# Kernel optimization log

Hardware: AMD Instinct MI355X
Metric: run time of the kernel (lower is better)

## Reference

```python
import jax, jax.numpy as jnp
import numpy as np

B, T, D, H = 2, 2048, 2048, 16
HD = D // H  # head dim = 128


def setup_inputs() -> dict:
    key = jax.random.key(0)
    k_x, k_qkv, k_out, k_doc = jax.random.split(key, 4)
    x = jax.random.normal(k_x, (B, T, D), dtype=jnp.float32)
    # real RoPE tables (sin/cos of position * inv_freq), shape (T, HD)
    inv_freq = 1.0 / (10000.0 ** (jnp.arange(0, HD, 2, dtype=jnp.float32) / HD))
    ang = jnp.arange(T, dtype=jnp.float32)[:, None] * inv_freq[None, :]  # (T, HD/2)
    ang = jnp.concatenate([ang, ang], axis=-1)  # (T, HD)
    sin, cos = jnp.sin(ang), jnp.cos(ang)
    W_qkv = jax.random.normal(k_qkv, (D, 3 * D), dtype=jnp.float32) * 0.02
    W_out = jax.random.normal(k_out, (D, D), dtype=jnp.float32) * 0.02
    # sorted doc ids per row -> contiguous packed documents
    doc_ids = jnp.sort(jax.random.randint(k_doc, (B, T), 0, 8), axis=-1).astype(jnp.int32)
    return {"x": x, "sin": sin, "cos": cos, "W_qkv": W_qkv, "W_out": W_out, "doc_ids": doc_ids}


def _apply_rope(xh, sin, cos):
    # xh: (B, T, H, HD); sin/cos: (T, HD) broadcast over batch & heads
    s = sin[None, :, None, :]
    c = cos[None, :, None, :]
    x1, x2 = jnp.split(xh, 2, axis=-1)
    rot = jnp.concatenate([-x2, x1], axis=-1)  # rotate_half
    return xh * c + rot * s


def reference(x, sin, cos, W_qkv, W_out, doc_ids):
    b, t, d = x.shape
    qkv = x @ W_qkv  # (B, T, 3D), fused QKV projection, no bias
    q, k, v = jnp.split(qkv, 3, axis=-1)
    q = q.reshape(b, t, H, HD)
    k = k.reshape(b, t, H, HD)
    v = v.reshape(b, t, H, HD)
    q = _apply_rope(q, sin, cos)
    k = _apply_rope(k, sin, cos)
    # doc-causal additive bias: (B, 1, T, T)
    neg_inf = jnp.finfo(q.dtype).min / 2
    causal = jnp.tril(jnp.ones((t, t), dtype=jnp.bool_))
    same_doc = doc_ids[:, :, None] == doc_ids[:, None, :]
    mask = (causal[None, :, :] & same_doc)[:, None, :, :]
    bias = jnp.where(mask, 0.0, neg_inf).astype(q.dtype)
    # attention (matches jax.nn.dot_product_attention with additive bias)
    scale = 1.0 / jnp.sqrt(jnp.asarray(HD, dtype=q.dtype))
    scores = jnp.einsum("bqhd,bkhd->bhqk", q, k) * scale + bias
    attn = jax.nn.softmax(scores, axis=-1)
    out = jnp.einsum("bhqk,bkhd->bqhd", attn, v)  # (B, T, H, HD)
    out = out.reshape(b, t, d)
    return out @ W_out
```

## Files before the change

kernel.cpp:

```cpp
#include <hip/hip_runtime.h>
#include <hip/hip_bf16.h>

#define BB 2
#define TT 2048
#define DD 2048
#define HH 16
#define HDIM 128
#define BT 4096
#define N3 6144

typedef __attribute__((ext_vector_type(8))) short s16x8;
typedef __attribute__((ext_vector_type(4))) float f32x4;

static __device__ __forceinline__ ushort f2bf(float x) {
  union { float f; unsigned u; } cv; cv.f = x;
  unsigned r = cv.u + 0x7FFF + ((cv.u >> 16) & 1);
  return (ushort)(r >> 16);
}
static __device__ __forceinline__ float bf2f(ushort u) {
  union { unsigned u; float f; } cv; cv.u = ((unsigned)u) << 16; return cv.f;
}

#define GLDS16(gp, lp) __builtin_amdgcn_global_load_lds( \
    (const __attribute__((address_space(1))) void*)(gp), \
    (__attribute__((address_space(3))) void*)(lp), 16, 0, 0)

__global__ void cvt_kernel(const float* __restrict__ in, ushort* __restrict__ out, int n4) {
  int i = blockIdx.x * blockDim.x + threadIdx.x;
  if (i < n4) {
    float4 v = ((const float4*)in)[i];
    ushort4 o;
    o.x = f2bf(v.x); o.y = f2bf(v.y); o.z = f2bf(v.z); o.w = f2bf(v.w);
    ((ushort4*)out)[i] = o;
  }
}

__global__ void transpose_cvt(const float* __restrict__ in, ushort* __restrict__ out, int R, int C) {
  __shared__ float tile[32][33];
  const int bx = blockIdx.x * 32, by = blockIdx.y * 32;
  const int tx = threadIdx.x, ty = threadIdx.y;
  #pragma unroll
  for (int i = 0; i < 32; i += 8)
    tile[ty + i][tx] = in[(size_t)(by + ty + i) * C + bx + tx];
  __syncthreads();
  #pragma unroll
  for (int i = 0; i < 32; i += 8)
    out[(size_t)(bx + ty + i) * R + by + tx] = f2bf(tile[tx][ty + i]);
}

__global__ __launch_bounds__(512, 1)
void gemm8_qkv(const ushort* __restrict__ A, const ushort* __restrict__ Bt,
               ushort* __restrict__ Qb, ushort* __restrict__ Kb, ushort* __restrict__ Vb)
{
  constexpr int K = 2048;
  constexpr int NT = K / 64;
  constexpr int NBX = N3 / 256;
  constexpr int NWG = NBX * (BT / 256);
  __shared__ char smem[131072];

  const int tid = threadIdx.x, wave = tid >> 6, lane = tid & 63;
  const int lr = lane & 15, lg = lane >> 4;
  const int wm = wave >> 2, wn = wave & 3;

  const int wg = blockIdx.x;
  const int nw = (wg & 7) * (NWG / 8) + (wg >> 3);
  const int by = nw / NBX, bx = nw - by * NBX;
  const int m0 = by * 256, n0 = bx * 256;

  auto STAGE = [&](int s) {
    if (s >= 4 * NT) return;
    const int U = s >> 2, j = s & 3;
    const int ab = j & 1, ks = j >> 1;
    const ushort* src = ab ? Bt : A;
    const int base0 = ab ? n0 : m0;
    char* dst = smem + (((U & 1) << 16) | (ab << 15) | (ks << 14));
    #pragma unroll
    for (int inst = 0; inst < 2; ++inst) {
      const int c = inst * 512 + tid;
      const int row = c >> 2;
      const int colb = (c & 3) * 16;
      const int colsw = colb ^ (((row >> 2) & 3) << 4);
      const ushort* gp = src + (size_t)(base0 + row) * K + U * 64 + ks * 32 + (colsw >> 1);
      GLDS16(gp, dst + inst * 8192 + wave * 1024);
    }
  };

  f32x4 acc[8][4] = {};

  #pragma unroll
  for (int s = 0; s < 6; ++s) STAGE(s);
  asm volatile("s_waitcnt vmcnt(8)" ::: "memory");
  __builtin_amdgcn_s_barrier();

  for (int T = 0; T < NT; ++T) {
    const int buf = T & 1;
    s16x8 a[8];
    #pragma unroll
    for (int p = 0; p < 4; ++p) {
      const int ks = p >> 1, qn = p & 1;
      const char* Ab = smem + ((buf << 16) | (ks << 14));
      const char* Bb = smem + ((buf << 16) | 32768 | (ks << 14));
      if ((p & 1) == 0) {
        #pragma unroll
        for (int mf = 0; mf < 8; ++mf) {
          const int row = wm * 128 + mf * 16 + lr;
          a[mf] = *(const s16x8*)(Ab + row * 64 + ((lg * 16) ^ (((row >> 2) & 3) << 4)));
        }
      }
      s16x8 bb[2];
      #pragma unroll
      for (int nf = 0; nf < 2; ++nf) {
        const int row = wn * 64 + qn * 32 + nf * 16 + lr;
        bb[nf] = *(const s16x8*)(Bb + row * 64 + ((lg * 16) ^ (((row >> 2) & 3) << 4)));
      }
      STAGE(4 * T + p + 6);
      if (p & 1) asm volatile("s_waitcnt vmcnt(8)" ::: "memory");
      __builtin_amdgcn_s_barrier();
      asm volatile("s_waitcnt lgkmcnt(0)" ::: "memory");
      __builtin_amdgcn_sched_barrier(0);
      __builtin_amdgcn_s_setprio(1);
      #pragma unroll
      for (int mf = 0; mf < 8; ++mf)
        #pragma unroll
        for (int nf = 0; nf < 2; ++nf)
          acc[mf][qn * 2 + nf] =
            __builtin_amdgcn_mfma_f32_16x16x32_bf16(a[mf], bb[nf], acc[mf][qn * 2 + nf], 0, 0, 0);
      __builtin_amdgcn_s_setprio(0);
      __builtin_amdgcn_s_barrier();
    }
  }

  #pragma unroll
  for (int mf = 0; mf < 8; ++mf) {
    #pragma unroll
    for (int nn = 0; nn < 4; ++nn) {
      #pragma unroll
      for (int r = 0; r < 4; ++r) {
        const int rowg = m0 + wm * 128 + mf * 16 + lg * 4 + r;
        const int colg = n0 + wn * 64 + nn * 16 + lr;
        const int which = colg >> 11, rem = colg & 2047;
        const int hh = rem >> 7, d = rem & 127;
        const int b2 = rowg >> 11, t = rowg & 2047;
        ushort* dstp = (which == 0) ? Qb : (which == 1) ? Kb : Vb;
        dstp[(((size_t)b2 * HH + hh) * TT + t) * HDIM + d] = f2bf(acc[mf][nn][r]);
      }
    }
  }
}

__global__ __launch_bounds__(256, 2)
void gemm_bt2(const ushort* __restrict__ A, const ushort* __restrict__ Bt,
              float* __restrict__ Cf, int M, int N, int K)
{
  __shared__ ushort As[128 * 32];
  __shared__ ushort Bs[128 * 32];
  const int tid = threadIdx.x;
  const int wave = tid >> 6, lane = tid & 63;
  const int lr = lane & 15, lg = lane >> 4;
  const int m0 = blockIdx.y * 128, n0 = blockIdx.x * 128;
  const int wm = (wave & 1) * 64, wn = (wave >> 1) * 64;
  f32x4 acc[4][4] = {};

  for (int k0 = 0; k0 < K; k0 += 32) {
    __syncthreads();
    #pragma unroll
    for (int call = 0; call < 2; ++call) {
      const int base = call * 256 + wave * 64;
      const int c = base + lane;
      const int row = c >> 2, cc = c & 3;
      GLDS16(A  + (size_t)(m0 + row) * K + k0 + cc * 8, As + (size_t)base * 8);
      GLDS16(Bt + (size_t)(n0 + row) * K + k0 + cc * 8, Bs + (size_t)base * 8);
    }
    __syncthreads();
    s16x8 a[4], b[4];
    #pragma unroll
    for (int i = 0; i < 4; ++i) a[i] = *(const s16x8*)&As[(wm + i * 16 + lr) * 32 + lg * 8];
    #pragma unroll
    for (int i = 0; i < 4; ++i) b[i] = *(const s16x8*)&Bs[(wn + i * 16 + lr) * 32 + lg * 8];
    #pragma unroll
    for (int mi = 0; mi < 4; ++mi)
      #pragma unroll
      for (int ni = 0; ni < 4; ++ni)
        acc[mi][ni] = __builtin_amdgcn_mfma_f32_16x16x32_bf16(a[mi], b[ni], acc[mi][ni], 0, 0, 0);
  }

  #pragma unroll
  for (int mi = 0; mi < 4; ++mi)
    #pragma unroll
    for (int ni = 0; ni < 4; ++ni)
      #pragma unroll
      for (int r = 0; r < 4; ++r) {
        const int row = m0 + wm + mi * 16 + lg * 4 + r;
        const int col = n0 + wn + ni * 16 + lr;
        Cf[(size_t)row * N + col] = acc[mi][ni][r];
      }
}

__global__ void rope_inplace(ushort* __restrict__ Qb, ushort* __restrict__ Kb,
                             const float* __restrict__ sinp, const float* __restrict__ cosp) {
  const int idx = blockIdx.x * 256 + threadIdx.x;
  const int d = idx & 63;
  const int t = (idx >> 6) & (TT - 1);
  const int bh = idx >> 17;
  const float c = cosp[t * HDIM + d];
  const float s = sinp[t * HDIM + d];
  const size_t base = ((size_t)bh * TT + t) * HDIM + d;
  float q1 = bf2f(Qb[base]), q2 = bf2f(Qb[base + 64]);
  Qb[base]      = f2bf(q1 * c - q2 * s);
  Qb[base + 64] = f2bf(q2 * c + q1 * s);
  float k1 = bf2f(Kb[base]), k2 = bf2f(Kb[base + 64]);
  Kb[base]      = f2bf(k1 * c - k2 * s);
  Kb[base + 64] = f2bf(k2 * c + k1 * s);
}

__global__ __launch_bounds__(256, 2)
void attn_kernel(const ushort* __restrict__ Qb, const ushort* __restrict__ Kb,
                 const ushort* __restrict__ Vb, const int* __restrict__ doc,
                 ushort* __restrict__ Ob)
{
  __shared__ ushort Ks[64 * 128];
  __shared__ ushort VTs[128 * 64];
  __shared__ ushort Ps[4][16 * 64];
  const int qt = blockIdx.x, h = blockIdx.y, b = blockIdx.z;
  const int q0 = qt * 64;
  const int tid = threadIdx.x, wave = tid >> 6, lane = tid & 63;
  const int lr = lane & 15, lg = lane >> 4;
  const size_t bh = (size_t)b * HH + h;
  const int* docb = doc + b * TT;

  const ushort* Qp = Qb + (bh * TT + q0 + wave * 16) * HDIM;
  s16x8 aq[4];
  #pragma unroll
  for (int ks = 0; ks < 4; ++ks) aq[ks] = *(const s16x8*)&Qp[lr * HDIM + ks * 32 + lg * 8];

  int qdoc[4];
  #pragma unroll
  for (int r = 0; r < 4; ++r) qdoc[r] = docb[q0 + wave * 16 + lg * 4 + r];
  const int qdoc0 = docb[q0];

  float m2[4], lsum[4];
  #pragma unroll
  for (int r = 0; r < 4; ++r) { m2[r] = -1e30f; lsum[r] = 0.f; }
  f32x4 oacc[8] = {};

  const float sc = 0.08838834764831843f * 1.4426950408889634f;

  const ushort* Kbase = Kb + bh * TT * HDIM;
  const ushort* Vbase = Vb + bh * TT * HDIM;

  const int ntiles = qt + 1;
  for (int kt = 0; kt < ntiles; ++kt) {
    const int kv0 = kt * 64;
    if (docb[kv0 + 63] < qdoc0) continue;
    __syncthreads();
    #pragma unroll
    for (int i = 0; i < 4; ++i) {
      const int c = tid + i * 256;
      const int row = c >> 4, c8 = c & 15;
      s16x8 v = *(const s16x8*)&Kbase[(size_t)(kv0 + row) * HDIM + c8 * 8];
      const int off = (row * 256 + c8 * 16) ^ ((row & 7) << 4);
      *(s16x8*)((char*)Ks + off) = v;
    }
    #pragma unroll
    for (int i = 0; i < 4; ++i) {
      const int c = tid + i * 256;
      const int kv = c >> 4, d8 = c & 15;
      s16x8 v = *(const s16x8*)&Vbase[(size_t)(kv0 + kv) * HDIM + d8 * 8];
      #pragma unroll
      for (int j = 0; j < 8; ++j) {
        const int d = d8 * 8 + j;
        const int off = (d * 128 + kv * 2) ^ ((d & 7) << 4);
        *(ushort*)((char*)VTs + off) = (ushort)v[j];
      }
    }
    __syncthreads();

    f32x4 sfrag[4] = {};
    #pragma unroll
    for (int ks = 0; ks < 4; ++ks) {
      #pragma unroll
      for (int ct = 0; ct < 4; ++ct) {
        const int row = ct * 16 + lr;
        const int off = (row * 256 + ks * 64 + lg * 16) ^ ((row & 7) << 4);
        s16x8 bk = *(const s16x8*)((char*)Ks + off);
        sfrag[ct] = __builtin_amdgcn_mfma_f32_16x16x32_bf16(aq[ks], bk, sfrag[ct], 0, 0, 0);
      }
    }

    int kd[4];
    #pragma unroll
    for (int ct = 0; ct < 4; ++ct) kd[ct] = docb[kv0 + ct * 16 + lr];

    float s[4][4], tmax[4];
    #pragma unroll
    for (int r = 0; r < 4; ++r) tmax[r] = -1e30f;
    #pragma unroll
    for (int ct = 0; ct < 4; ++ct) {
      const int col = kv0 + ct * 16 + lr;
      #pragma unroll
      for (int r = 0; r < 4; ++r) {
        const int row = q0 + wave * 16 + lg * 4 + r;
        float v = sfrag[ct][r] * sc;
        const bool keep = (col <= row) && (kd[ct] == qdoc[r]);
        v = keep ? v : -1e30f;
        s[ct][r] = v;
        tmax[r] = fmaxf(tmax[r], v);
      }
    }
    #pragma unroll
    for (int r = 0; r < 4; ++r) {
      #pragma unroll
      for (int off = 8; off >= 1; off >>= 1)
        tmax[r] = fmaxf(tmax[r], __shfl_xor(tmax[r], off, 16));
    }
    float alpha[4];
    #pragma unroll
    for (int r = 0; r < 4; ++r) {
      const float mnew = fmaxf(m2[r], tmax[r]);
      alpha[r] = exp2f(m2[r] - mnew);
      m2[r] = mnew;
      lsum[r] *= alpha[r];
    }
    #pragma unroll
    for (int ct = 0; ct < 4; ++ct) {
      #pragma unroll
      for (int r = 0; r < 4; ++r) {
        const float p = (s[ct][r] > -1e29f) ? exp2f(s[ct][r] - m2[r]) : 0.f;
        lsum[r] += p;
        const int prow = lg * 4 + r;
        const int off = (prow * 128 + (ct * 16 + lr) * 2) ^ ((prow & 7) << 4);
        *(ushort*)((char*)&Ps[wave][0] + off) = f2bf(p);
      }
    }
    #pragma unroll
    for (int oc = 0; oc < 8; ++oc)
      #pragma unroll
      for (int r = 0; r < 4; ++r) oacc[oc][r] *= alpha[r];
    #pragma unroll
    for (int ks = 0; ks < 2; ++ks) {
      const int poff = (lr * 128 + ks * 64 + lg * 16) ^ ((lr & 7) << 4);
      s16x8 ap = *(const s16x8*)((char*)&Ps[wave][0] + poff);
      #pragma unroll
      for (int oc = 0; oc < 8; ++oc) {
        const int vrow = oc * 16 + lr;
        const int voff = (vrow * 128 + ks * 64 + lg * 16) ^ ((vrow & 7) << 4);
        s16x8 bv = *(const s16x8*)((char*)VTs + voff);
        oacc[oc] = __builtin_amdgcn_mfma_f32_16x16x32_bf16(ap, bv, oacc[oc], 0, 0, 0);
      }
    }
  }

  #pragma unroll
  for (int r = 0; r < 4; ++r)
    #pragma unroll
    for (int off = 8; off >= 1; off >>= 1)
      lsum[r] += __shfl_xor(lsum[r], off, 16);

  ushort* Op = Ob + ((size_t)b * TT + q0 + wave * 16) * DD + (size_t)h * HDIM;
  #pragma unroll
  for (int oc = 0; oc < 8; ++oc)
    #pragma unroll
    for (int r = 0; r < 4; ++r)
      Op[(lg * 4 + r) * DD + oc * 16 + lr] = f2bf(oacc[oc][r] / lsum[r]);
}

extern "C" void kernel_launch(void* const* d_in, const int* in_sizes, int n_in,
                              void* d_out, int out_size, void* d_ws, size_t ws_size,
                              hipStream_t stream)
{
  const float* x    = (const float*)d_in[0];
  const float* sinp = (const float*)d_in[1];
  const float* cosp = (const float*)d_in[2];
  const float* Wqkv = (const float*)d_in[3];
  const float* Wout = (const float*)d_in[4];
  const int*   doc  = (const int*)d_in[5];
  float* out = (float*)d_out;

  ushort* xb  = (ushort*)d_ws;
  ushort* WqT = xb  + (size_t)BT * DD;
  ushort* WoT = WqT + (size_t)N3 * DD;
  ushort* Qb  = WoT + (size_t)DD * DD;
  ushort* Kb  = Qb  + (size_t)BB * TT * DD;
  ushort* Vb  = Kb  + (size_t)BB * TT * DD;
  ushort* Ob  = Vb  + (size_t)BB * TT * DD;

  cvt_kernel<<<(BT * DD / 4 + 255) / 256, 256, 0, stream>>>(x, xb, BT * DD / 4);
  transpose_cvt<<<dim3(N3 / 32, DD / 32), dim3(32, 8), 0, stream>>>(Wqkv, WqT, DD, N3);
  transpose_cvt<<<dim3(DD / 32, DD / 32), dim3(32, 8), 0, stream>>>(Wout, WoT, DD, DD);
  gemm8_qkv<<<dim3((N3 / 256) * (BT / 256)), 512, 0, stream>>>(xb, WqT, Qb, Kb, Vb);
  rope_inplace<<<BB * HH * TT * 64 / 256, 256, 0, stream>>>(Qb, Kb, sinp, cosp);
  attn_kernel<<<dim3(TT / 64, HH, BB), 256, 0, stream>>>(Qb, Kb, Vb, doc, Ob);
  gemm_bt2<<<dim3(DD / 128, BT / 128), 256, 0, stream>>>(Ob, WoT, out, BT, DD, DD);
}
```

Measured before the change: 406.3 us.

## Restructure QKV GEMM staging into full-K tile loads and regroup workgroup-to-tile mapping

After: 407.6 us. No clear change (+0.3%).

```diff
diff --git a/kernel.cpp b/kernel.cpp
--- a/kernel.cpp
+++ b/kernel.cpp
@@ -54,8 +54,6 @@
 {
   constexpr int K = 2048;
   constexpr int NT = K / 64;
-  constexpr int NBX = N3 / 256;
-  constexpr int NWG = NBX * (BT / 256);
   __shared__ char smem[131072];
 
   const int tid = threadIdx.x, wave = tid >> 6, lane = tid & 63;
@@ -63,58 +61,55 @@
   const int wm = wave >> 2, wn = wave & 3;
 
   const int wg = blockIdx.x;
-  const int nw = (wg & 7) * (NWG / 8) + (wg >> 3);
-  const int by = nw / NBX, bx = nw - by * NBX;
+  const int xcd = wg & 7, l = wg >> 3;
+  const int rgrp = xcd >> 2, cgrp = xcd & 3;
+  const int lrow = l & 7, lcol = l >> 3;
+  const int by = rgrp * 8 + lrow, bx = cgrp * 6 + lcol;
   const int m0 = by * 256, n0 = bx * 256;
 
-  auto STAGE = [&](int s) {
-    if (s >= 4 * NT) return;
-    const int U = s >> 2, j = s & 3;
-    const int ab = j & 1, ks = j >> 1;
-    const ushort* src = ab ? Bt : A;
-    const int base0 = ab ? n0 : m0;
-    char* dst = smem + (((U & 1) << 16) | (ab << 15) | (ks << 14));
-    #pragma unroll
-    for (int inst = 0; inst < 2; ++inst) {
+  auto stage2 = [&](const ushort* src, int base0, int U, char* region) {
+    #pragma unroll
+    for (int inst = 0; inst < 4; ++inst) {
       const int c = inst * 512 + tid;
-      const int row = c >> 2;
-      const int colb = (c & 3) * 16;
-      const int colsw = colb ^ (((row >> 2) & 3) << 4);
-      const ushort* gp = src + (size_t)(base0 + row) * K + U * 64 + ks * 32 + (colsw >> 1);
-      GLDS16(gp, dst + inst * 8192 + wave * 1024);
+      const int row = c >> 3;
+      const int colb = (c & 7) * 16;
+      const int colsw = colb ^ (((row >> 2) & 1) << 5);
+      const ushort* gp = src + (size_t)(base0 + row) * K + U * 64 + (colsw >> 1);
+      GLDS16(gp, region + inst * 8192 + wave * 1024);
     }
   };
 
   f32x4 acc[8][4] = {};
 
-  #pragma unroll
-  for (int s = 0; s < 6; ++s) STAGE(s);
-  asm volatile("s_waitcnt vmcnt(8)" ::: "memory");
+  stage2(A,  m0, 0, smem);
+  stage2(Bt, n0, 0, smem + 32768);
+  stage2(A,  m0, 1, smem + 65536);
+  asm volatile("s_waitcnt vmcnt(4)" ::: "memory");
   __builtin_amdgcn_s_barrier();
 
   for (int T = 0; T < NT; ++T) {
     const int buf = T & 1;
+    char* Ab = smem + (buf << 16);
+    char* Bb = smem + (buf << 16) + 32768;
     s16x8 a[8];
     #pragma unroll
     for (int p = 0; p < 4; ++p) {
-      const int ks = p >> 1, qn = p & 1;
-      const char* Ab = smem + ((buf << 16) | (ks << 14));
-      const char* Bb = smem + ((buf << 16) | 32768 | (ks << 14));
+      const int kk = p >> 1, qn = p & 1;
       if ((p & 1) == 0) {
         #pragma unroll
         for (int mf = 0; mf < 8; ++mf) {
-          const int row = wm * 128 + mf * 16 + lr;
-          a[mf] = *(const s16x8*)(Ab + row * 64 + ((lg * 16) ^ (((row >> 2) & 3) << 4)));
+          const int r = wm * 128 + mf * 16 + lr;
+          a[mf] = *(const s16x8*)(Ab + r * 128 + ((kk * 64 + lg * 16) ^ (((r >> 2) & 1) << 5)));
         }
       }
-      s16x8 bb[2];
+      s16x8 b[2];
       #pragma unroll
       for (int nf = 0; nf < 2; ++nf) {
-        const int row = wn * 64 + qn * 32 + nf * 16 + lr;
-        bb[nf] = *(const s16x8*)(Bb + row * 64 + ((lg * 16) ^ (((row >> 2) & 3) << 4)));
-      }
-      STAGE(4 * T + p + 6);
-      if (p & 1) asm volatile("s_waitcnt vmcnt(8)" ::: "memory");
+        const int r = wn * 64 + (qn * 2 + nf) * 16 + lr;
+        b[nf] = *(const s16x8*)(Bb + r * 128 + ((kk * 64 + lg * 16) ^ (((r >> 2) & 1) << 5)));
+      }
+      if (p == 0 && T + 1 < NT) stage2(Bt, n0, T + 1, smem + (((T + 1) & 1) << 16) + 32768);
+      if (p == 3 && T + 2 < NT) stage2(A,  m0, T + 2, smem + ((buf) << 16));
       __builtin_amdgcn_s_barrier();
       asm volatile("s_waitcnt lgkmcnt(0)" ::: "memory");
       __builtin_amdgcn_sched_barrier(0);
@@ -124,8 +119,12 @@
         #pragma unroll
         for (int nf = 0; nf < 2; ++nf)
           acc[mf][qn * 2 + nf] =
-            __builtin_amdgcn_mfma_f32_16x16x32_bf16(a[mf], bb[nf], acc[mf][qn * 2 + nf], 0, 0, 0);
+            __builtin_amdgcn_mfma_f32_16x16x32_bf16(a[mf], b[nf], acc[mf][qn * 2 + nf], 0, 0, 0);
       __builtin_amdgcn_s_setprio(0);
+      if (p == 3) {
+        if (T < NT - 2) { asm volatile("s_waitcnt vmcnt(4)" ::: "memory"); }
+        else            { asm volatile("s_waitcnt vmcnt(0)" ::: "memory"); }
+      }
       __builtin_amdgcn_s_barrier();
     }
   }
```
